# Kernel tuning notes

Hardware: AMD Instinct MI355X
Metric: run time of the kernel (lower is better)

Reference implementation:

```python
import jax, jax.numpy as jnp
import numpy as np

N, FEATURES, CODES, PAGES = 32768, 768, 64, 8192
BETA = 0.25


def _normalise(x):
    return x / jnp.linalg.norm(x, axis=-1, keepdims=True)


def setup_inputs() -> dict:
    key = jax.random.key(0)
    k_z, k_wi, k_wo, k_cb = jax.random.split(key, 4)
    return {
        "z": jax.random.normal(k_z, (N, FEATURES), dtype=jnp.float32),
        "w_in": jax.random.normal(k_wi, (CODES, FEATURES), dtype=jnp.float32) * 0.02,
        "b_in": jnp.zeros((CODES,), dtype=jnp.float32),
        "w_out": jax.random.normal(k_wo, (FEATURES, CODES), dtype=jnp.float32) * 0.02,
        "b_out": jnp.zeros((FEATURES,), dtype=jnp.float32),
        "codebook": jax.random.normal(k_cb, (PAGES, CODES), dtype=jnp.float32),
    }


def reference(z, w_in, b_in, w_out, b_out, codebook):
    sg = jax.lax.stop_gradient
    # project + L2-normalise samples and codes
    zq = _normalise(z @ w_in.T + b_in)          # [n, codes]
    cn = _normalise(codebook)                   # [pages, codes]
    # squared euclidean distance without materialising [n, pages, codes]:
    # ||z||^2 + ||c||^2 - 2 z c^T
    d = (
        jnp.sum(zq * zq, axis=-1, keepdims=True)
        + jnp.sum(cn * cn, axis=-1)[None, :]
        - 2.0 * (zq @ cn.T)
    )                                           # [n, pages]
    idxes = jnp.argmin(d, axis=-1)              # [n]
    codes = _normalise(codebook[idxes])         # lookup then normalise, as in source
    loss = BETA * jnp.mean((sg(zq) - codes) ** 2) + jnp.mean((zq - sg(codes)) ** 2)
    codes = zq + sg(codes - zq)                 # straight-through
    out = codes @ w_out.T + b_out               # [n, features]
    return out, loss, idxes
```

## Files before the change

### kernel.cpp

```cpp
#include <hip/hip_runtime.h>

#define N 32768
#define F 768
#define C 64
#define P 8192
#define TAU 1e-3f

typedef __attribute__((ext_vector_type(8))) short short8;
typedef __attribute__((ext_vector_type(4))) float f32x4;

#define WS_CNT    0
#define WS_CC     (WS_CNT + C*P)
#define WS_ZQT    (WS_CC + P)
#define WS_CODEST (WS_ZQT + C*N)
#define WS_WIH    WS_CODEST
#define WS_WIM    (WS_WIH + (C*F)/2)
#define WS_WIL    (WS_WIM + (C*F)/2)
#define WS_IDX    (WS_CODEST + C*N)
#define WS_QN     (WS_IDX + N)
#define WS_ACC    (WS_QN + 1)
#define WS_QLIST  (WS_ACC + 1)
#define WS_CNH    ((WS_QLIST + N + 3) & ~3)
#define WS_CNL    (WS_CNH + (C*P)/2)
#define WS_ZQH    (WS_CNL + (C*P)/2)
#define WS_ZQL    (WS_ZQH + (C*N)/2)
#define WS_D12    (WS_ZQL + (C*N)/2)
#define WS_WOH    (WS_D12 + 16*N)
#define WS_WOL    (WS_WOH + (F*C)/2)

#define OUT_LOSS_OFF (N*F)
#define OUT_IDX_OFF  (N*F + 1)

__device__ inline unsigned short f2bf(float x) {
    union { float f; unsigned u; } v; v.f = x;
    unsigned r = v.u + 0x7fffu + ((v.u >> 16) & 1u);
    return (unsigned short)(r >> 16);
}
__device__ inline float bf2f(unsigned short b) {
    union { unsigned u; float f; } v; v.u = ((unsigned)b) << 16;
    return v.f;
}

union U32S8 { unsigned u[4]; short8 s; };

__device__ inline void split3x8(const float* xp, short8& h, short8& m, short8& l) {
    U32S8 hh, mm, ll;
#pragma unroll
    for (int i = 0; i < 4; ++i) {
        float xa = xp[2 * i], xb = xp[2 * i + 1];
        unsigned ha = __float_as_uint(xa) & 0xffff0000u;
        unsigned hb = __float_as_uint(xb) & 0xffff0000u;
        hh.u[i] = (ha >> 16) | hb;
        float ra = xa - __uint_as_float(ha), rb = xb - __uint_as_float(hb);
        unsigned ma = __float_as_uint(ra) & 0xffff0000u;
        unsigned mb = __float_as_uint(rb) & 0xffff0000u;
        mm.u[i] = (ma >> 16) | mb;
        float sa = ra - __uint_as_float(ma), sb = rb - __uint_as_float(mb);
        ll.u[i] = ((__float_as_uint(sa) & 0xffff0000u) >> 16) |
                  (__float_as_uint(sb) & 0xffff0000u);
    }
    h = hh.s; m = mm.s; l = ll.s;
}

__global__ __launch_bounds__(256) void k1_norm_codebook(
    const float* __restrict__ cb, float* __restrict__ cnT, float* __restrict__ cc,
    unsigned short* __restrict__ cnh, unsigned short* __restrict__ cnl) {
    int p = blockIdx.x * 256 + threadIdx.x;
    const float4* cb4 = (const float4*)(cb + (size_t)p * C);
    float4 v[16];
    float ss = 0.f;
#pragma unroll
    for (int i = 0; i < 16; ++i) {
        v[i] = cb4[i];
        ss += v[i].x * v[i].x + v[i].y * v[i].y + v[i].z * v[i].z + v[i].w * v[i].w;
    }
    float nrm = sqrtf(ss);
    float s2 = 0.f;
    unsigned short hb[64], lb[64];
#pragma unroll
    for (int i = 0; i < 16; ++i) {
        float c4[4] = {v[i].x / nrm, v[i].y / nrm, v[i].z / nrm, v[i].w / nrm};
#pragma unroll
        for (int j = 0; j < 4; ++j) {
            cnT[(size_t)(i * 4 + j) * P + p] = c4[j];
            s2 += c4[j] * c4[j];
            unsigned short h = f2bf(c4[j]);
            hb[i * 4 + j] = h;
            lb[i * 4 + j] = f2bf(c4[j] - bf2f(h));
        }
    }
    cc[p] = s2;
#pragma unroll
    for (int i = 0; i < 8; ++i) {
        uint4 hv, lv;
        hv.x = (unsigned)hb[i*8+0] | ((unsigned)hb[i*8+1] << 16);
        hv.y = (unsigned)hb[i*8+2] | ((unsigned)hb[i*8+3] << 16);
        hv.z = (unsigned)hb[i*8+4] | ((unsigned)hb[i*8+5] << 16);
        hv.w = (unsigned)hb[i*8+6] | ((unsigned)hb[i*8+7] << 16);
        lv.x = (unsigned)lb[i*8+0] | ((unsigned)lb[i*8+1] << 16);
        lv.y = (unsigned)lb[i*8+2] | ((unsigned)lb[i*8+3] << 16);
        lv.z = (unsigned)lb[i*8+4] | ((unsigned)lb[i*8+5] << 16);
        lv.w = (unsigned)lb[i*8+6] | ((unsigned)lb[i*8+7] << 16);
        *(uint4*)&cnh[(size_t)p * 64 + i * 8] = hv;
        *(uint4*)&cnl[(size_t)p * 64 + i * 8] = lv;
    }
}

__global__ __launch_bounds__(256) void k2_prep(
    const float* __restrict__ w_in, unsigned short* __restrict__ wih,
    unsigned short* __restrict__ wim, unsigned short* __restrict__ wil) {
    int i = blockIdx.x * 256 + threadIdx.x;
    float x = w_in[i];
    unsigned hu = __float_as_uint(x) & 0xffff0000u;
    float r1 = x - __uint_as_float(hu);
    unsigned mu = __float_as_uint(r1) & 0xffff0000u;
    float r2 = r1 - __uint_as_float(mu);
    wih[i] = (unsigned short)(hu >> 16);
    wim[i] = (unsigned short)(mu >> 16);
    wil[i] = f2bf(r2);
}

__global__ __launch_bounds__(64) void k2_project_mfma(
    const float* __restrict__ z,
    const unsigned short* __restrict__ wih, const unsigned short* __restrict__ wim,
    const unsigned short* __restrict__ wil, const float* __restrict__ b_in,
    float* __restrict__ zqT, unsigned short* __restrict__ zqh,
    unsigned short* __restrict__ zql) {
    __shared__ float lq[16 * 65];
    int lane = threadIdx.x;
    int col = lane & 15, quad = lane >> 4;
    int wrow = blockIdx.x * 16;

    f32x4 acc[4];
#pragma unroll
    for (int nt = 0; nt < 4; ++nt) acc[nt] = (f32x4){0.f, 0.f, 0.f, 0.f};

    const float* zrow = z + (size_t)(wrow + col) * F + quad * 8;
    size_t bbase[4];
#pragma unroll
    for (int nt = 0; nt < 4; ++nt) bbase[nt] = (size_t)(nt * 16 + col) * F + quad * 8;

#pragma unroll 2
    for (int kt = 0; kt < F / 32; ++kt) {
        float xz[8];
        *(float4*)&xz[0] = *(const float4*)&zrow[kt * 32];
        *(float4*)&xz[4] = *(const float4*)&zrow[kt * 32 + 4];
        short8 ah, am, al;
        split3x8(xz, ah, am, al);
#pragma unroll
        for (int nt = 0; nt < 4; ++nt) {
            size_t bo = bbase[nt] + kt * 32;
            short8 bh = *(const short8*)&wih[bo];
            short8 bm = *(const short8*)&wim[bo];
            short8 bl = *(const short8*)&wil[bo];
            acc[nt] = __builtin_amdgcn_mfma_f32_16x16x32_bf16(ah, bh, acc[nt], 0, 0, 0);
            acc[nt] = __builtin_amdgcn_mfma_f32_16x16x32_bf16(ah, bm, acc[nt], 0, 0, 0);
            acc[nt] = __builtin_amdgcn_mfma_f32_16x16x32_bf16(am, bh, acc[nt], 0, 0, 0);
            acc[nt] = __builtin_amdgcn_mfma_f32_16x16x32_bf16(ah, bl, acc[nt], 0, 0, 0);
            acc[nt] = __builtin_amdgcn_mfma_f32_16x16x32_bf16(al, bh, acc[nt], 0, 0, 0);
            acc[nt] = __builtin_amdgcn_mfma_f32_16x16x32_bf16(am, bm, acc[nt], 0, 0, 0);
        }
    }
    float y[4][4];
#pragma unroll
    for (int nt = 0; nt < 4; ++nt) {
        float bv = b_in[nt * 16 + col];
#pragma unroll
        for (int s = 0; s < 4; ++s) y[nt][s] = acc[nt][s] + bv;
    }
#pragma unroll
    for (int s = 0; s < 4; ++s) {
        float ssum = 0.f;
#pragma unroll
        for (int nt = 0; nt < 4; ++nt) ssum += y[nt][s] * y[nt][s];
#pragma unroll
        for (int m = 1; m <= 8; m <<= 1) ssum += __shfl_xor(ssum, m);
        float nrm = sqrtf(ssum);
#pragma unroll
        for (int nt = 0; nt < 4; ++nt) y[nt][s] /= nrm;
    }
#pragma unroll
    for (int nt = 0; nt < 4; ++nt)
#pragma unroll
        for (int s = 0; s < 4; ++s)
            lq[(quad * 4 + s) * 65 + nt * 16 + col] = y[nt][s];
    __syncthreads();
    {
        int r = lane >> 2, part = lane & 3;
        float v[16];
#pragma unroll
        for (int t = 0; t < 16; ++t) v[t] = lq[r * 65 + part * 16 + t];
        unsigned hu[8], lu[8];
#pragma unroll
        for (int k = 0; k < 8; ++k) {
            unsigned short h0 = f2bf(v[2 * k]), h1 = f2bf(v[2 * k + 1]);
            unsigned short l0 = f2bf(v[2 * k] - bf2f(h0));
            unsigned short l1 = f2bf(v[2 * k + 1] - bf2f(h1));
            hu[k] = (unsigned)h0 | ((unsigned)h1 << 16);
            lu[k] = (unsigned)l0 | ((unsigned)l1 << 16);
        }
        size_t ro = (size_t)(wrow + r) * 64 + part * 16;
        *(uint4*)&zqh[ro] = make_uint4(hu[0], hu[1], hu[2], hu[3]);
        *(uint4*)&zqh[ro + 8] = make_uint4(hu[4], hu[5], hu[6], hu[7]);
        *(uint4*)&zql[ro] = make_uint4(lu[0], lu[1], lu[2], lu[3]);
        *(uint4*)&zql[ro + 8] = make_uint4(lu[4], lu[5], lu[6], lu[7]);
    }
    {
        float t[16];
#pragma unroll
        for (int r = 0; r < 16; ++r) t[r] = lq[r * 65 + lane];
        float* dst = &zqT[(size_t)lane * N + wrow];
#pragma unroll
        for (int g = 0; g < 4; ++g)
            *(float4*)&dst[g * 4] = make_float4(t[4 * g], t[4 * g + 1], t[4 * g + 2], t[4 * g + 3]);
    }
}

__global__ __launch_bounds__(256, 4) void k3_argmin_mfma(
    const unsigned short* __restrict__ zqh, const unsigned short* __restrict__ zql,
    const unsigned short* __restrict__ cnh, const unsigned short* __restrict__ cnl,
    float4* __restrict__ d12) {
    __shared__ unsigned short lfrag[8 * 4 * 64 * 8];
    int tid = threadIdx.x;
    int w = tid >> 6, lane = tid & 63;
    int col = lane & 15, quad = lane >> 4;
    int rb = (blockIdx.x & 255) * 128;
    int ph = blockIdx.x >> 8;
    int wrow = rb + w * 32;
    int p0 = ph * (P / 4);

    short8 ah[2][2], al[2][2];
#pragma unroll
    for (int mm = 0; mm < 2; ++mm)
#pragma unroll
        for (int kf = 0; kf < 2; ++kf) {
            size_t off = (size_t)(wrow + mm * 16 + col) * 64 + kf * 32 + quad * 8;
            ah[mm][kf] = *(const short8*)&zqh[off];
            al[mm][kf] = *(const short8*)&zql[off];
        }

    float s1[8], s2[8]; int i1[8];
#pragma unroll
    for (int r = 0; r < 8; ++r) { s1[r] = -3.4e38f; s2[r] = -3.4e38f; i1[r] = 0; }

    int sq = (tid >> 4) & 3, scol = tid & 15, sf = w;
    const unsigned short* ssrc = (sf & 2) ? cnl : cnh;
    int skf = sf & 1;

    for (int pt = p0; pt < p0 + P / 4; pt += 128) {
        __syncthreads();
#pragma unroll
        for (int nt = 0; nt < 8; ++nt) {
            int p = pt + nt * 16 + scol;
            uint4 dv = *(const uint4*)&ssrc[(size_t)p * 64 + skf * 32 + sq * 8];
            *(uint4*)&lfrag[((nt * 4 + sf) * 64 + (tid & 63)) * 8] = dv;
        }
        __syncthreads();
#pragma unroll 2
        for (int nt = 0; nt < 8; ++nt) {
            short8 bh0 = *(const short8*)&lfrag[((nt * 4 + 0) * 64 + lane) * 8];
            short8 bh1 = *(const short8*)&lfrag[((nt * 4 + 1) * 64 + lane) * 8];
            short8 bl0 = *(const short8*)&lfrag[((nt * 4 + 2) * 64 + lane) * 8];
            short8 bl1 = *(const short8*)&lfrag[((nt * 4 + 3) * 64 + lane) * 8];
            int p = pt + nt * 16 + col;
#pragma unroll
            for (int mm = 0; mm < 2; ++mm) {
                f32x4 acc = {0.f, 0.f, 0.f, 0.f};
                acc = __builtin_amdgcn_mfma_f32_16x16x32_bf16(ah[mm][0], bh0, acc, 0, 0, 0);
                acc = __builtin_amdgcn_mfma_f32_16x16x32_bf16(ah[mm][1], bh1, acc, 0, 0, 0);
                acc = __builtin_amdgcn_mfma_f32_16x16x32_bf16(ah[mm][0], bl0, acc, 0, 0, 0);
                acc = __builtin_amdgcn_mfma_f32_16x16x32_bf16(ah[mm][1], bl1, acc, 0, 0, 0);
                acc = __builtin_amdgcn_mfma_f32_16x16x32_bf16(al[mm][0], bh0, acc, 0, 0, 0);
                acc = __builtin_amdgcn_mfma_f32_16x16x32_bf16(al[mm][1], bh1, acc, 0, 0, 0);
#pragma unroll
                for (int s = 0; s < 4; ++s) {
                    float sv = acc[s];
                    int r = mm * 4 + s;
                    bool gt = sv > s1[r];
                    i1[r] = gt ? p : i1[r];
                    s2[r] = fmaxf(s2[r], fminf(s1[r], sv));
                    s1[r] = fmaxf(s1[r], sv);
                }
            }
        }
    }
#pragma unroll
    for (int r = 0; r < 8; ++r) {
        float a1v = s1[r], a2v = s2[r]; int ai = i1[r];
#pragma unroll
        for (int m = 1; m <= 8; m <<= 1) {
            float b1 = __shfl_xor(a1v, m); int bi = __shfl_xor(ai, m);
            float b2 = __shfl_xor(a2v, m);
            float n1 = fmaxf(a1v, b1);
            a2v = fmaxf(fminf(a1v, b1), fmaxf(a2v, b2));
            ai = (b1 > a1v) ? bi : ai;
            a1v = n1;
        }
        if (col == 0) {
            int row = wrow + (r >> 2) * 16 + quad * 4 + (r & 3);
            d12[ph * N + row] = make_float4(a1v, a2v, __int_as_float(ai), 0.f);
        }
    }
}

__global__ __launch_bounds__(256) void k3m_merge(
    const float4* __restrict__ d12, int* __restrict__ idx_ws, float* __restrict__ idx_out,
    int* __restrict__ qn, int* __restrict__ qlist) {
    int row = blockIdx.x * 256 + threadIdx.x;
    float4 a = d12[row];
    float m1 = a.x, m2 = a.y; int i1 = __float_as_int(a.z);
#pragma unroll
    for (int ph = 1; ph < 4; ++ph) {
        float4 b = d12[ph * N + row];
        m2 = fmaxf(fminf(m1, b.x), fmaxf(m2, b.y));
        if (b.x > m1) { i1 = __float_as_int(b.z); m1 = b.x; }
    }
    idx_ws[row] = i1;
    idx_out[row] = (float)i1;
    if (m1 - m2 < 0.5f * TAU + 2e-6f) {
        int qi = atomicAdd(qn, 1);
        qlist[qi] = row;
    }
}

__global__ __launch_bounds__(256) void k3_recheck(
    const float* __restrict__ zqT, const float* __restrict__ cnT,
    const float* __restrict__ cc, const int* __restrict__ qn,
    const int* __restrict__ qlist, int* __restrict__ idx_ws, float* __restrict__ idx_out) {
    __shared__ float zrow[64];
    __shared__ float bv[4];
    __shared__ int   bi4[4];
    int tid = threadIdx.x, w = tid >> 6, lane = tid & 63;
    int nq = qn[0];
    for (int e = blockIdx.x; e < nq; e += gridDim.x) {
        int row = qlist[e];
        __syncthreads();
        if (tid < 64) zrow[tid] = zqT[(size_t)tid * N + row];
        __syncthreads();
        float best = 3.4e38f; int bp = 0;
        for (int pb = w * 2048; pb < (w + 1) * 2048; pb += 64) {
            int p = pb + lane;
            float a0 = 0.f, a1 = 0.f, a2 = 0.f, a3 = 0.f;
#pragma unroll
            for (int k = 0; k < 64; k += 4) {
                a0 = fmaf(zrow[k + 0], cnT[(size_t)(k + 0) * P + p], a0);
                a1 = fmaf(zrow[k + 1], cnT[(size_t)(k + 1) * P + p], a1);
                a2 = fmaf(zrow[k + 2], cnT[(size_t)(k + 2) * P + p], a2);
                a3 = fmaf(zrow[k + 3], cnT[(size_t)(k + 3) * P + p], a3);
            }
            float d = fmaf((a0 + a1) + (a2 + a3), -2.0f, cc[p]);
            if (d < best) { best = d; bp = p; }
        }
#pragma unroll
        for (int m = 1; m < 64; m <<= 1) {
            float ob = __shfl_xor(best, m); int op = __shfl_xor(bp, m);
            if (ob < best || (ob == best && op < bp)) { best = ob; bp = op; }
        }
        if (lane == 0) { bv[w] = best; bi4[w] = bp; }
        __syncthreads();
        if (tid == 0) {
            float b = bv[0]; int pi = bi4[0];
#pragma unroll
            for (int ww = 1; ww < 4; ++ww)
                if (bv[ww] < b || (bv[ww] == b && bi4[ww] < pi)) { b = bv[ww]; pi = bi4[ww]; }
            idx_ws[row] = pi; idx_out[row] = (float)pi;
        }
    }
}

__global__ __launch_bounds__(256) void k3b_gather_loss(
    const float* __restrict__ cnT, const int* __restrict__ idx,
    const float* __restrict__ zqT, float* __restrict__ acc) {
    float s = 0.f;
    for (size_t i = (size_t)blockIdx.x * 256 + threadIdx.x; i < (size_t)C * N;
         i += (size_t)gridDim.x * 256) {
        int k = (int)(i >> 15);
        int r = (int)(i & (N - 1));
        float d = zqT[i] - cnT[(size_t)k * P + idx[r]];
        s = fmaf(d, d, s);
    }
#pragma unroll
    for (int off = 32; off > 0; off >>= 1) s += __shfl_xor(s, off);
    __shared__ float wsum[4];
    int lane = threadIdx.x & 63, wv = threadIdx.x >> 6;
    if (lane == 0) wsum[wv] = s;
    __syncthreads();
    if (threadIdx.x == 0) atomicAdd(acc, wsum[0] + wsum[1] + wsum[2] + wsum[3]);
}

__global__ __launch_bounds__(256) void k4_prep(
    const float* __restrict__ w_out, unsigned short* __restrict__ woh,
    unsigned short* __restrict__ wol) {
    int i = blockIdx.x * 256 + threadIdx.x;
    float v = w_out[i];
    unsigned short h = f2bf(v);
    woh[i] = h;
    wol[i] = f2bf(v - bf2f(h));
}

__global__ __launch_bounds__(256) void k4_out_mfma(
    const unsigned short* __restrict__ cnh, const unsigned short* __restrict__ cnl,
    const unsigned short* __restrict__ woh, const unsigned short* __restrict__ wol,
    const int* __restrict__ idx, const float* __restrict__ b_out, float* __restrict__ out) {
    int tid = threadIdx.x;
    int w = tid >> 6, lane = tid & 63;
    int col = lane & 15, quad = lane >> 4;
    int rb = (blockIdx.x >> 2) * 64;
    int fb = (blockIdx.x & 3) * 192;
    int wrow = rb + w * 16;

    int pg = idx[wrow + col];
    short8 ah[2], al[2];
#pragma unroll
    for (int kf = 0; kf < 2; ++kf) {
        size_t off = (size_t)pg * 64 + kf * 32 + quad * 8;
        ah[kf] = *(const short8*)&cnh[off];
        al[kf] = *(const short8*)&cnl[off];
    }

    for (int ft = 0; ft < 12; ++ft) {
        int f0 = fb + ft * 16;
        size_t bo = (size_t)(f0 + col) * 64 + quad * 8;
        short8 bh0 = *(const short8*)&woh[bo];
        short8 bh1 = *(const short8*)&woh[bo + 32];
        short8 bl0 = *(const short8*)&wol[bo];
        short8 bl1 = *(const short8*)&wol[bo + 32];
        f32x4 acc = {0.f, 0.f, 0.f, 0.f};
        acc = __builtin_amdgcn_mfma_f32_16x16x32_bf16(ah[0], bh0, acc, 0, 0, 0);
        acc = __builtin_amdgcn_mfma_f32_16x16x32_bf16(ah[1], bh1, acc, 0, 0, 0);
        acc = __builtin_amdgcn_mfma_f32_16x16x32_bf16(ah[0], bl0, acc, 0, 0, 0);
        acc = __builtin_amdgcn_mfma_f32_16x16x32_bf16(ah[1], bl1, acc, 0, 0, 0);
        acc = __builtin_amdgcn_mfma_f32_16x16x32_bf16(al[0], bh0, acc, 0, 0, 0);
        acc = __builtin_amdgcn_mfma_f32_16x16x32_bf16(al[1], bh1, acc, 0, 0, 0);
        float bv = b_out[f0 + col];
#pragma unroll
        for (int s = 0; s < 4; ++s)
            out[(size_t)(wrow + quad * 4 + s) * F + f0 + col] = acc[s] + bv;
    }
}

__global__ void k6_finalize(const float* __restrict__ acc, float* __restrict__ loss_out) {
    float m = acc[0] / (float)(C * N);
    loss_out[0] = 0.25f * m + m;
}

extern "C" void kernel_launch(void* const* d_in, const int* in_sizes, int n_in,
                              void* d_out, int out_size, void* d_ws, size_t ws_size,
                              hipStream_t stream) {
    const float* z      = (const float*)d_in[0];
    const float* w_in   = (const float*)d_in[1];
    const float* b_in   = (const float*)d_in[2];
    const float* w_out  = (const float*)d_in[3];
    const float* b_out  = (const float*)d_in[4];
    const float* cb     = (const float*)d_in[5];
    float* out = (float*)d_out;
    float* ws  = (float*)d_ws;

    unsigned short* cnh = (unsigned short*)(ws + WS_CNH);
    unsigned short* cnl = (unsigned short*)(ws + WS_CNL);
    unsigned short* zqh = (unsigned short*)(ws + WS_ZQH);
    unsigned short* zql = (unsigned short*)(ws + WS_ZQL);
    unsigned short* woh = (unsigned short*)(ws + WS_WOH);
    unsigned short* wol = (unsigned short*)(ws + WS_WOL);
    unsigned short* wih = (unsigned short*)(ws + WS_WIH);
    unsigned short* wim = (unsigned short*)(ws + WS_WIM);
    unsigned short* wil = (unsigned short*)(ws + WS_WIL);

    hipMemsetAsync(ws + WS_QN, 0, 2 * sizeof(float), stream);
    k1_norm_codebook<<<P / 256, 256, 0, stream>>>(cb, ws + WS_CNT, ws + WS_CC, cnh, cnl);
    k2_prep<<<C * F / 256, 256, 0, stream>>>(w_in, wih, wim, wil);
    k4_prep<<<F * C / 256, 256, 0, stream>>>(w_out, woh, wol);
    k2_project_mfma<<<N / 16, 64, 0, stream>>>(z, wih, wim, wil, b_in,
                                               ws + WS_ZQT, zqh, zql);
    k3_argmin_mfma<<<1024, 256, 0, stream>>>(zqh, zql, cnh, cnl, (float4*)(ws + WS_D12));
    k3m_merge<<<N / 256, 256, 0, stream>>>((const float4*)(ws + WS_D12),
                                           (int*)(ws + WS_IDX), out + OUT_IDX_OFF,
                                           (int*)(ws + WS_QN), (int*)(ws + WS_QLIST));
    k3_recheck<<<512, 256, 0, stream>>>(ws + WS_ZQT, ws + WS_CNT, ws + WS_CC,
                                        (const int*)(ws + WS_QN), (const int*)(ws + WS_QLIST),
                                        (int*)(ws + WS_IDX), out + OUT_IDX_OFF);
    k3b_gather_loss<<<2048, 256, 0, stream>>>(ws + WS_CNT, (const int*)(ws + WS_IDX),
                                              ws + WS_ZQT, ws + WS_ACC);
    k4_out_mfma<<<2048, 256, 0, stream>>>(cnh, cnl, woh, wol, (const int*)(ws + WS_IDX),
                                          b_out, out);
    k6_finalize<<<1, 1, 0, stream>>>(ws + WS_ACC, out + OUT_LOSS_OFF);
}
```

Before: 529.2 us.

## Split projection K across waves, widen argmin row tiles, batch recheck rows

The projection kernel now uses two waves per block, each covering half of the K dimension, and reduces their partial sums in shared memory before normalising. The argmin kernel gives each wave 64 rows instead of 32, so every codebook fragment held in LDS is reused by more rows. The page range is split into 8 phases instead of 4, the merge kernel reads 8 partials, and the running second-best uses a med3 instruction. The recheck kernel handles 8 queued rows per block, so each codebook load feeds 8 dot products. The wider tiles raise register pressure, which the launch bound of 3 blocks per CU reflects, and the D12 buffer is moved into the workspace region the w_in splits also use.

```diff
diff --git a/kernel.cpp b/kernel.cpp
--- a/kernel.cpp
+++ b/kernel.cpp
@@ -16,6 +16,7 @@
 #define WS_WIH    WS_CODEST
 #define WS_WIM    (WS_WIH + (C*F)/2)
 #define WS_WIL    (WS_WIM + (C*F)/2)
+#define WS_D12    (WS_WIL + (C*F)/2)
 #define WS_IDX    (WS_CODEST + C*N)
 #define WS_QN     (WS_IDX + N)
 #define WS_ACC    (WS_QN + 1)
@@ -24,8 +25,7 @@
 #define WS_CNL    (WS_CNH + (C*P)/2)
 #define WS_ZQH    (WS_CNL + (C*P)/2)
 #define WS_ZQL    (WS_ZQH + (C*N)/2)
-#define WS_D12    (WS_ZQL + (C*N)/2)
-#define WS_WOH    (WS_D12 + 16*N)
+#define WS_WOH    (WS_ZQL + (C*N)/2)
 #define WS_WOL    (WS_WOH + (F*C)/2)
 
 #define OUT_LOSS_OFF (N*F)
@@ -120,14 +120,15 @@
     wil[i] = f2bf(r2);
 }
 
-__global__ __launch_bounds__(64) void k2_project_mfma(
+__global__ __launch_bounds__(128) void k2_project_mfma(
     const float* __restrict__ z,
     const unsigned short* __restrict__ wih, const unsigned short* __restrict__ wim,
     const unsigned short* __restrict__ wil, const float* __restrict__ b_in,
     float* __restrict__ zqT, unsigned short* __restrict__ zqh,
     unsigned short* __restrict__ zql) {
-    __shared__ float lq[16 * 65];
-    int lane = threadIdx.x;
+    __shared__ float lacc[2][16][68];
+    int tid = threadIdx.x;
+    int w = tid >> 6, lane = tid & 63;
     int col = lane & 15, quad = lane >> 4;
     int wrow = blockIdx.x * 16;
 
@@ -136,12 +137,8 @@
     for (int nt = 0; nt < 4; ++nt) acc[nt] = (f32x4){0.f, 0.f, 0.f, 0.f};
 
     const float* zrow = z + (size_t)(wrow + col) * F + quad * 8;
-    size_t bbase[4];
-#pragma unroll
-    for (int nt = 0; nt < 4; ++nt) bbase[nt] = (size_t)(nt * 16 + col) * F + quad * 8;
-
 #pragma unroll 2
-    for (int kt = 0; kt < F / 32; ++kt) {
+    for (int kt = w * 12; kt < w * 12 + 12; ++kt) {
         float xz[8];
         *(float4*)&xz[0] = *(const float4*)&zrow[kt * 32];
         *(float4*)&xz[4] = *(const float4*)&zrow[kt * 32 + 4];
@@ -149,7 +146,7 @@
         split3x8(xz, ah, am, al);
 #pragma unroll
         for (int nt = 0; nt < 4; ++nt) {
-            size_t bo = bbase[nt] + kt * 32;
+            size_t bo = (size_t)(nt * 16 + col) * F + kt * 32 + quad * 8;
             short8 bh = *(const short8*)&wih[bo];
             short8 bm = *(const short8*)&wim[bo];
             short8 bl = *(const short8*)&wil[bo];
@@ -161,62 +158,57 @@
             acc[nt] = __builtin_amdgcn_mfma_f32_16x16x32_bf16(am, bm, acc[nt], 0, 0, 0);
         }
     }
-    float y[4][4];
-#pragma unroll
-    for (int nt = 0; nt < 4; ++nt) {
-        float bv = b_in[nt * 16 + col];
-#pragma unroll
-        for (int s = 0; s < 4; ++s) y[nt][s] = acc[nt][s] + bv;
-    }
-#pragma unroll
-    for (int s = 0; s < 4; ++s) {
-        float ssum = 0.f;
-#pragma unroll
-        for (int nt = 0; nt < 4; ++nt) ssum += y[nt][s] * y[nt][s];
-#pragma unroll
-        for (int m = 1; m <= 8; m <<= 1) ssum += __shfl_xor(ssum, m);
-        float nrm = sqrtf(ssum);
-#pragma unroll
-        for (int nt = 0; nt < 4; ++nt) y[nt][s] /= nrm;
-    }
 #pragma unroll
     for (int nt = 0; nt < 4; ++nt)
 #pragma unroll
         for (int s = 0; s < 4; ++s)
-            lq[(quad * 4 + s) * 65 + nt * 16 + col] = y[nt][s];
+            lacc[w][quad * 4 + s][nt * 16 + col] = acc[nt][s];
+    __syncthreads();
+    int row = tid >> 3, cg = tid & 7;
+    float y[8];
+#pragma unroll
+    for (int j = 0; j < 8; ++j) {
+        int c = cg * 8 + j;
+        y[j] = lacc[0][row][c] + lacc[1][row][c] + b_in[c];
+    }
+    float ssum = 0.f;
+#pragma unroll
+    for (int j = 0; j < 8; ++j) ssum += y[j] * y[j];
+#pragma unroll
+    for (int m = 1; m <= 4; m <<= 1) ssum += __shfl_xor(ssum, m);
+    float nrm = sqrtf(ssum);
+#pragma unroll
+    for (int j = 0; j < 8; ++j) y[j] /= nrm;
+    {
+        unsigned hu[4], lu[4];
+#pragma unroll
+        for (int k = 0; k < 4; ++k) {
+            unsigned short h0 = f2bf(y[2 * k]), h1 = f2bf(y[2 * k + 1]);
+            unsigned short l0 = f2bf(y[2 * k] - bf2f(h0));
+            unsigned short l1 = f2bf(y[2 * k + 1] - bf2f(h1));
+            hu[k] = (unsigned)h0 | ((unsigned)h1 << 16);
+            lu[k] = (unsigned)l0 | ((unsigned)l1 << 16);
+        }
+        size_t ro = (size_t)(wrow + row) * 64 + cg * 8;
+        *(uint4*)&zqh[ro] = make_uint4(hu[0], hu[1], hu[2], hu[3]);
+        *(uint4*)&zql[ro] = make_uint4(lu[0], lu[1], lu[2], lu[3]);
+    }
+    __syncthreads();
+#pragma unroll
+    for (int j = 0; j < 8; ++j) lacc[0][row][cg * 8 + j] = y[j];
     __syncthreads();
     {
-        int r = lane >> 2, part = lane & 3;
-        float v[16];
-#pragma unroll
-        for (int t = 0; t < 16; ++t) v[t] = lq[r * 65 + part * 16 + t];
-        unsigned hu[8], lu[8];
-#pragma unroll
-        for (int k = 0; k < 8; ++k) {
-            unsigned short h0 = f2bf(v[2 * k]), h1 = f2bf(v[2 * k + 1]);
-            unsigned short l0 = f2bf(v[2 * k] - bf2f(h0));
-            unsigned short l1 = f2bf(v[2 * k + 1] - bf2f(h1));
-            hu[k] = (unsigned)h0 | ((unsigned)h1 << 16);
-            lu[k] = (unsigned)l0 | ((unsigned)l1 << 16);
-        }
-        size_t ro = (size_t)(wrow + r) * 64 + part * 16;
-        *(uint4*)&zqh[ro] = make_uint4(hu[0], hu[1], hu[2], hu[3]);
-        *(uint4*)&zqh[ro + 8] = make_uint4(hu[4], hu[5], hu[6], hu[7]);
-        *(uint4*)&zql[ro] = make_uint4(lu[0], lu[1], lu[2], lu[3]);
-        *(uint4*)&zql[ro + 8] = make_uint4(lu[4], lu[5], lu[6], lu[7]);
-    }
-    {
-        float t[16];
-#pragma unroll
-        for (int r = 0; r < 16; ++r) t[r] = lq[r * 65 + lane];
-        float* dst = &zqT[(size_t)lane * N + wrow];
-#pragma unroll
-        for (int g = 0; g < 4; ++g)
-            *(float4*)&dst[g * 4] = make_float4(t[4 * g], t[4 * g + 1], t[4 * g + 2], t[4 * g + 3]);
-    }
-}
-
-__global__ __launch_bounds__(256, 4) void k3_argmin_mfma(
+        int c = tid & 63, half = tid >> 6;
+        float t[8];
+#pragma unroll
+        for (int r = 0; r < 8; ++r) t[r] = lacc[0][half * 8 + r][c];
+        float* dst = &zqT[(size_t)c * N + wrow + half * 8];
+        *(float4*)&dst[0] = make_float4(t[0], t[1], t[2], t[3]);
+        *(float4*)&dst[4] = make_float4(t[4], t[5], t[6], t[7]);
+    }
+}
+
+__global__ __launch_bounds__(256, 3) void k3_argmin_mfma(
     const unsigned short* __restrict__ zqh, const unsigned short* __restrict__ zql,
     const unsigned short* __restrict__ cnh, const unsigned short* __restrict__ cnl,
     float4* __restrict__ d12) {
@@ -224,14 +216,14 @@
     int tid = threadIdx.x;
     int w = tid >> 6, lane = tid & 63;
     int col = lane & 15, quad = lane >> 4;
-    int rb = (blockIdx.x & 255) * 128;
-    int ph = blockIdx.x >> 8;
-    int wrow = rb + w * 32;
-    int p0 = ph * (P / 4);
-
-    short8 ah[2][2], al[2][2];
-#pragma unroll
-    for (int mm = 0; mm < 2; ++mm)
+    int rb = (blockIdx.x & 127) * 256;
+    int ph = blockIdx.x >> 7;
+    int wrow = rb + w * 64;
+    int p0 = ph * (P / 8);
+
+    short8 ah[4][2], al[4][2];
+#pragma unroll
+    for (int mm = 0; mm < 4; ++mm)
 #pragma unroll
         for (int kf = 0; kf < 2; ++kf) {
             size_t off = (size_t)(wrow + mm * 16 + col) * 64 + kf * 32 + quad * 8;
@@ -239,15 +231,15 @@
             al[mm][kf] = *(const short8*)&zql[off];
         }
 
-    float s1[8], s2[8]; int i1[8];
-#pragma unroll
-    for (int r = 0; r < 8; ++r) { s1[r] = -3.4e38f; s2[r] = -3.4e38f; i1[r] = 0; }
+    float s1[16], s2[16]; int i1[16];
+#pragma unroll
+    for (int r = 0; r < 16; ++r) { s1[r] = -3.4e38f; s2[r] = -3.4e38f; i1[r] = 0; }
 
     int sq = (tid >> 4) & 3, scol = tid & 15, sf = w;
     const unsigned short* ssrc = (sf & 2) ? cnl : cnh;
     int skf = sf & 1;
 
-    for (int pt = p0; pt < p0 + P / 4; pt += 128) {
+    for (int pt = p0; pt < p0 + P / 8; pt += 128) {
         __syncthreads();
 #pragma unroll
         for (int nt = 0; nt < 8; ++nt) {
@@ -256,7 +248,7 @@
             *(uint4*)&lfrag[((nt * 4 + sf) * 64 + (tid & 63)) * 8] = dv;
         }
         __syncthreads();
-#pragma unroll 2
+#pragma unroll 1
         for (int nt = 0; nt < 8; ++nt) {
             short8 bh0 = *(const short8*)&lfrag[((nt * 4 + 0) * 64 + lane) * 8];
             short8 bh1 = *(const short8*)&lfrag[((nt * 4 + 1) * 64 + lane) * 8];
@@ -264,7 +256,7 @@
             short8 bl1 = *(const short8*)&lfrag[((nt * 4 + 3) * 64 + lane) * 8];
             int p = pt + nt * 16 + col;
 #pragma unroll
-            for (int mm = 0; mm < 2; ++mm) {
+            for (int mm = 0; mm < 4; ++mm) {
                 f32x4 acc = {0.f, 0.f, 0.f, 0.f};
                 acc = __builtin_amdgcn_mfma_f32_16x16x32_bf16(ah[mm][0], bh0, acc, 0, 0, 0);
                 acc = __builtin_amdgcn_mfma_f32_16x16x32_bf16(ah[mm][1], bh1, acc, 0, 0, 0);
@@ -278,14 +270,14 @@
                     int r = mm * 4 + s;
                     bool gt = sv > s1[r];
                     i1[r] = gt ? p : i1[r];
-                    s2[r] = fmaxf(s2[r], fminf(s1[r], sv));
+                    s2[r] = __builtin_amdgcn_fmed3f(s1[r], sv, s2[r]);
                     s1[r] = fmaxf(s1[r], sv);
                 }
             }
         }
     }
 #pragma unroll
-    for (int r = 0; r < 8; ++r) {
+    for (int r = 0; r < 16; ++r) {
         float a1v = s1[r], a2v = s2[r]; int ai = i1[r];
 #pragma unroll
         for (int m = 1; m <= 8; m <<= 1) {
@@ -310,7 +302,7 @@
     float4 a = d12[row];
     float m1 = a.x, m2 = a.y; int i1 = __float_as_int(a.z);
 #pragma unroll
-    for (int ph = 1; ph < 4; ++ph) {
+    for (int ph = 1; ph < 8; ++ph) {
         float4 b = d12[ph * N + row];
         m2 = fmaxf(fminf(m1, b.x), fmaxf(m2, b.y));
         if (b.x > m1) { i1 = __float_as_int(b.z); m1 = b.x; }
@@ -327,43 +319,67 @@
     const float* __restrict__ zqT, const float* __restrict__ cnT,
     const float* __restrict__ cc, const int* __restrict__ qn,
     const int* __restrict__ qlist, int* __restrict__ idx_ws, float* __restrict__ idx_out) {
-    __shared__ float zrow[64];
-    __shared__ float bv[4];
-    __shared__ int   bi4[4];
+    __shared__ float zrT[64][8];
+    __shared__ float bv[4][8];
+    __shared__ int   bi[4][8];
+    __shared__ int   rows[8];
     int tid = threadIdx.x, w = tid >> 6, lane = tid & 63;
     int nq = qn[0];
-    for (int e = blockIdx.x; e < nq; e += gridDim.x) {
-        int row = qlist[e];
+    for (int g = blockIdx.x * 8; g < nq; g += gridDim.x * 8) {
+        int cnt = min(8, nq - g);
         __syncthreads();
-        if (tid < 64) zrow[tid] = zqT[(size_t)tid * N + row];
+        if (tid < 8) rows[tid] = (tid < cnt) ? qlist[g + tid] : 0;
         __syncthreads();
-        float best = 3.4e38f; int bp = 0;
+        for (int i = tid; i < 8 * 64; i += 256) {
+            int j = i & 7, k = i >> 3;
+            zrT[k][j] = (j < cnt) ? zqT[(size_t)k * N + rows[j]] : 0.f;
+        }
+        __syncthreads();
+        float best[8]; int bp[8];
+#pragma unroll
+        for (int j = 0; j < 8; ++j) { best[j] = 3.4e38f; bp[j] = 0; }
         for (int pb = w * 2048; pb < (w + 1) * 2048; pb += 64) {
             int p = pb + lane;
-            float a0 = 0.f, a1 = 0.f, a2 = 0.f, a3 = 0.f;
-#pragma unroll
-            for (int k = 0; k < 64; k += 4) {
-                a0 = fmaf(zrow[k + 0], cnT[(size_t)(k + 0) * P + p], a0);
-                a1 = fmaf(zrow[k + 1], cnT[(size_t)(k + 1) * P + p], a1);
-                a2 = fmaf(zrow[k + 2], cnT[(size_t)(k + 2) * P + p], a2);
-                a3 = fmaf(zrow[k + 3], cnT[(size_t)(k + 3) * P + p], a3);
+            float a[8];
+#pragma unroll
+            for (int j = 0; j < 8; ++j) a[j] = 0.f;
+#pragma unroll 4
+            for (int k = 0; k < 64; ++k) {
+                float cv = cnT[(size_t)k * P + p];
+                float4 z0 = *(const float4*)&zrT[k][0];
+                float4 z1 = *(const float4*)&zrT[k][4];
+                a[0] = fmaf(z0.x, cv, a[0]); a[1] = fmaf(z0.y, cv, a[1]);
+                a[2] = fmaf(z0.z, cv, a[2]); a[3] = fmaf(z0.w, cv, a[3]);
+                a[4] = fmaf(z1.x, cv, a[4]); a[5] = fmaf(z1.y, cv, a[5]);
+                a[6] = fmaf(z1.z, cv, a[6]); a[7] = fmaf(z1.w, cv, a[7]);
             }
-            float d = fmaf((a0 + a1) + (a2 + a3), -2.0f, cc[p]);
-            if (d < best) { best = d; bp = p; }
-        }
-#pragma unroll
-        for (int m = 1; m < 64; m <<= 1) {
-            float ob = __shfl_xor(best, m); int op = __shfl_xor(bp, m);
-            if (ob < best || (ob == best && op < bp)) { best = ob; bp = op; }
-        }
-        if (lane == 0) { bv[w] = best; bi4[w] = bp; }
+            float ccv = cc[p];
+#pragma unroll
+            for (int j = 0; j < 8; ++j) {
+                float d = fmaf(a[j], -2.0f, ccv);
+                if (d < best[j]) { best[j] = d; bp[j] = p; }
+            }
+        }
+#pragma unroll
+        for (int j = 0; j < 8; ++j) {
+#pragma unroll
+            for (int m = 1; m < 64; m <<= 1) {
+                float ob = __shfl_xor(best[j], m); int op = __shfl_xor(bp[j], m);
+                if (ob < best[j] || (ob == best[j] && op < bp[j])) { best[j] = ob; bp[j] = op; }
+            }
+        }
+        if (lane == 0) {
+#pragma unroll
+            for (int j = 0; j < 8; ++j) { bv[w][j] = best[j]; bi[w][j] = bp[j]; }
+        }
         __syncthreads();
-        if (tid == 0) {
-            float b = bv[0]; int pi = bi4[0];
+        if (tid < cnt) {
+            int j = tid;
+            float b = bv[0][j]; int pi = bi[0][j];
 #pragma unroll
             for (int ww = 1; ww < 4; ++ww)
-                if (bv[ww] < b || (bv[ww] == b && bi4[ww] < pi)) { b = bv[ww]; pi = bi4[ww]; }
-            idx_ws[row] = pi; idx_out[row] = (float)pi;
+                if (bv[ww][j] < b || (bv[ww][j] == b && bi[ww][j] < pi)) { b = bv[ww][j]; pi = bi[ww][j]; }
+            idx_ws[rows[j]] = pi; idx_out[rows[j]] = (float)pi;
         }
     }
 }
@@ -470,8 +486,8 @@
     k1_norm_codebook<<<P / 256, 256, 0, stream>>>(cb, ws + WS_CNT, ws + WS_CC, cnh, cnl);
     k2_prep<<<C * F / 256, 256, 0, stream>>>(w_in, wih, wim, wil);
     k4_prep<<<F * C / 256, 256, 0, stream>>>(w_out, woh, wol);
-    k2_project_mfma<<<N / 16, 64, 0, stream>>>(z, wih, wim, wil, b_in,
-                                               ws + WS_ZQT, zqh, zql);
+    k2_project_mfma<<<N / 16, 128, 0, stream>>>(z, wih, wim, wil, b_in,
+                                                ws + WS_ZQT, zqh, zql);
     k3_argmin_mfma<<<1024, 256, 0, stream>>>(zqh, zql, cnh, cnl, (float4*)(ws + WS_D12));
     k3m_merge<<<N / 256, 256, 0, stream>>>((const float4*)(ws + WS_D12),
                                            (int*)(ws + WS_IDX), out + OUT_IDX_OFF,
```

Result: slower. 662.3 us (+25.1%).
